# Optimization experiments

Hardware: AMD Instinct MI355X
Metric: run time of the kernel (lower is better)

## Reference

```python
import jax, jax.numpy as jnp
import numpy as np
import math

B, S, D, HD = 8, 2048, 768, 64  # batch, seq, emb_hidden_dim, head_dim


def setup_inputs() -> dict:
    key = jax.random.key(0)
    ks = jax.random.split(key, 7)
    scale_w = 1.0 / math.sqrt(D)
    return {
        "X": jax.random.normal(ks[0], (B, S, D), dtype=jnp.float32),
        "Wq": jax.random.normal(ks[1], (D, HD), dtype=jnp.float32) * scale_w,
        "bq": jax.random.normal(ks[2], (HD,), dtype=jnp.float32) * 0.01,
        "Wk": jax.random.normal(ks[3], (D, HD), dtype=jnp.float32) * scale_w,
        "bk": jax.random.normal(ks[4], (HD,), dtype=jnp.float32) * 0.01,
        "Wv": jax.random.normal(ks[5], (D, HD), dtype=jnp.float32) * scale_w,
        "bv": jax.random.normal(ks[6], (HD,), dtype=jnp.float32) * 0.01,
    }


def reference(X, Wq, bq, Wk, bk, Wv, bv):
    # Projections: [B,S,D] @ [D,HD] -> [B,S,HD]
    Q = X @ Wq + bq
    K = X @ Wk + bk
    V = X @ Wv + bv
    # NOTE: original divides by sqrt(hidden_dim)=sqrt(D), not sqrt(head_dim)
    inv_scale = 1.0 / math.sqrt(D)
    scores = jnp.einsum("bqd,bkd->bqk", Q, K) * inv_scale  # [B,S,S]
    causal = jnp.tril(jnp.ones((S, S), dtype=bool))
    scores = jnp.where(causal, scores, -jnp.inf)
    attn = jax.nn.softmax(scores, axis=-1)
    # dropout p=0.0 (eval/deterministic reference)
    return jnp.einsum("bqk,bkd->bqd", attn, V)  # [B,S,HD]
```

## Files before the change

### kernel.cpp

```cpp
#include <hip/hip_runtime.h>
#include <hip/hip_bf16.h>
#include <math.h>

typedef __attribute__((ext_vector_type(8))) short short8;
typedef __attribute__((ext_vector_type(4))) float f32x4;

#define SS 2048
#define DD 768
#define HDIM 64
#define MM 16384

__device__ __forceinline__ short f2bf(float f) {
    union { float f; unsigned u; } v; v.f = f;
    unsigned r = (v.u + 0x7fffu + ((v.u >> 16) & 1u)) >> 16;
    return (short)r;
}
__device__ __forceinline__ float bf2f(short s) {
    union { float f; unsigned u; } v;
    v.u = ((unsigned)(unsigned short)s) << 16;
    return v.f;
}

__device__ __forceinline__ void gl_lds(const void* g, void* l) {
    __builtin_amdgcn_global_load_lds(
        (const __attribute__((address_space(1))) unsigned*)g,
        (__attribute__((address_space(3))) unsigned*)l, 16, 0, 0);
}

__global__ void prep_w(const float* __restrict__ Wq, const float* __restrict__ Wk,
                       const float* __restrict__ Wv, short* __restrict__ Wt) {
    int idx = blockIdx.x * 256 + threadIdx.x;
    int col = idx / DD;
    int k   = idx - col * DD;
    const float* W = (col < 64) ? Wq : (col < 128) ? Wk : Wv;
    int c = col & 63;
    Wt[idx] = f2bf(W[k * HDIM + c]);
}

__global__ __launch_bounds__(512)
void proj_qkv(const float* __restrict__ X, const short* __restrict__ Wt,
              const float* __restrict__ bq, const float* __restrict__ bk,
              const float* __restrict__ bv,
              short* __restrict__ Qg, short* __restrict__ Kg, short* __restrict__ Vt) {
    __shared__ float Xl[2][2048];
    __shared__ short Wl[2][12288];
    const int tid = threadIdx.x;
    const int w = tid >> 6, lane = tid & 63;
    const int lr = lane & 15, lg = lane >> 4;
    const int wr = w >> 2, wc = w & 3;
    const int row0 = blockIdx.x * 32;

    f32x4 acc[3];
    #pragma unroll
    for (int cf = 0; cf < 3; cf++) acc[cf] = (f32x4)0.0f;

    auto stage = [&](int kk, int buf) {
        {
            int o = w * 1024 + lane * 16;
            int row = o >> 8, ch = (o >> 4) & 15;
            const char* src = (const char*)X + (size_t)(row0 + row) * 3072
                              + kk * 256 + ((ch ^ (row & 7)) << 4);
            gl_lds(src, (char*)&Xl[buf][0] + w * 1024);
        }
        #pragma unroll
        for (int s = 0; s < 3; s++) {
            int i = w * 3 + s;
            int o = i * 1024 + lane * 16;
            int col = o >> 7, ch = (o >> 4) & 7;
            const char* src = (const char*)Wt + (size_t)col * 1536
                              + kk * 128 + ((ch ^ (col & 7)) << 4);
            gl_lds(src, (char*)&Wl[buf][0] + i * 1024);
        }
    };

    stage(0, 0);
    __syncthreads();
    int buf = 0;
    for (int kk = 0; kk < 12; kk++) {
        if (kk < 11) stage(kk + 1, buf ^ 1);
        const char* xb = (const char*)&Xl[buf][0];
        const char* wb = (const char*)&Wl[buf][0];
        #pragma unroll
        for (int ksub = 0; ksub < 2; ksub++) {
            int r = wr * 16 + lr;
            int b0 = r * 256 + ksub * 128 + lg * 32;
            f32x4 x0 = *(const f32x4*)(xb + ((b0)      ^ ((r & 7) << 4)));
            f32x4 x1 = *(const f32x4*)(xb + ((b0 + 16) ^ ((r & 7) << 4)));
            short8 a;
            a[0]=f2bf(x0[0]); a[1]=f2bf(x0[1]); a[2]=f2bf(x0[2]); a[3]=f2bf(x0[3]);
            a[4]=f2bf(x1[0]); a[5]=f2bf(x1[1]); a[6]=f2bf(x1[2]); a[7]=f2bf(x1[3]);
            #pragma unroll
            for (int cf = 0; cf < 3; cf++) {
                int col = wc * 48 + cf * 16 + lr;
                short8 bfr = *(const short8*)(wb +
                    ((col * 128 + ksub * 64 + lg * 16) ^ ((col & 7) << 4)));
                acc[cf] = __builtin_amdgcn_mfma_f32_16x16x32_bf16(a, bfr, acc[cf], 0, 0, 0);
            }
        }
        __syncthreads();
        buf ^= 1;
    }

    #pragma unroll
    for (int cf = 0; cf < 3; cf++) {
        int gcol = wc * 48 + cf * 16 + lr;
        int m = gcol >> 6, cc = gcol & 63;
        float bias = (m == 0 ? bq : m == 1 ? bk : bv)[cc];
        #pragma unroll
        for (int i = 0; i < 4; i++) {
            int r = row0 + wr * 16 + lg * 4 + i;
            short o = f2bf(acc[cf][i] + bias);
            if (m == 0)      Qg[(size_t)r * HDIM + cc] = o;
            else if (m == 1) Kg[(size_t)r * HDIM + cc] = o;
            else             Vt[(size_t)cc * MM + r]   = o;
        }
    }
}

__global__ __launch_bounds__(512)
void attn_part(const short* __restrict__ Qg, const short* __restrict__ Kg,
               const short* __restrict__ Vt,
               short* __restrict__ Opart, float* __restrict__ Ml,
               float* __restrict__ out) {
    __shared__ short Kl[2][4096];
    __shared__ short Vl[2][4096];
    __shared__ short Pl[8][1024];
    const int tid = threadIdx.x;
    const int w = tid >> 6, lane = tid & 63;
    const int lr = lane & 15, lg = lane >> 4;
    const int b = blockIdx.y;

    int idx = 71 - (int)blockIdx.x;
    int g = 0;
    while (idx >= (g + 1) * (g + 2)) g++;
    int rem = idx - g * (g + 1);
    int jq = rem / (g + 1);
    const int J = 2 * g + jq;
    const int c = rem - jq * (g + 1);
    const int t0 = c * 4;
    const int t1 = min(2 * J + 2, t0 + 4);

    const int q0 = J * 128 + w * 16;
    char* plbase = (char*)&Pl[w][0];

    short8 qf[2];
    qf[0] = *(const short8*)(Qg + ((size_t)b * SS + q0 + lr) * HDIM + lg * 8);
    qf[1] = *(const short8*)(Qg + ((size_t)b * SS + q0 + lr) * HDIM + 32 + lg * 8);

    f32x4 oacc[4];
    #pragma unroll
    for (int d = 0; d < 4; d++) oacc[d] = (f32x4)0.0f;
    float mrow[4] = {-INFINITY, -INFINITY, -INFINITY, -INFINITY};
    float lrow[4] = {0.f, 0.f, 0.f, 0.f};
    const float scl = 0.03608439182435161f;

    auto stage = [&](int t, int buf) {
        const int kv0 = t * 64;
        {
            int o = w * 1024 + lane * 16;
            int row = o >> 7, ch = (o >> 4) & 7;
            const char* src = (const char*)Kg + ((size_t)b * SS + kv0) * 128
                              + row * 128 + ((ch ^ (row & 7)) << 4);
            gl_lds(src, (char*)&Kl[buf][0] + w * 1024);
        }
        {
            int o = w * 1024 + lane * 16;
            int col = o >> 7, ch = (o >> 4) & 7;
            const char* src = (const char*)Vt + (size_t)col * (MM * 2)
                              + ((size_t)b * SS + kv0) * 2 + ((ch ^ (col & 7)) << 4);
            gl_lds(src, (char*)&Vl[buf][0] + w * 1024);
        }
    };

    stage(t0, 0);
    __syncthreads();
    int buf = 0;
    for (int t = t0; t < t1; t++) {
        if (t + 1 < t1) stage(t + 1, buf ^ 1);
        const int kv0 = t * 64;
        const bool active = (kv0 <= q0 + 15);
        if (active) {
            const char* kb = (const char*)&Kl[buf][0];
            f32x4 sacc[4];
            #pragma unroll
            for (int ct = 0; ct < 4; ct++) sacc[ct] = (f32x4)0.0f;
            #pragma unroll
            for (int ct = 0; ct < 4; ct++) {
                int row = ct * 16 + lr;
                short8 k0 = *(const short8*)(kb + ((row * 128 +      lg * 16) ^ ((row & 7) << 4)));
                short8 k1 = *(const short8*)(kb + ((row * 128 + 64 + lg * 16) ^ ((row & 7) << 4)));
                sacc[ct] = __builtin_amdgcn_mfma_f32_16x16x32_bf16(qf[0], k0, sacc[ct], 0, 0, 0);
                sacc[ct] = __builtin_amdgcn_mfma_f32_16x16x32_bf16(qf[1], k1, sacc[ct], 0, 0, 0);
            }

            const bool maskt = (kv0 + 63 > q0);
            float p[4][4];
            float rm[4] = {-1e30f, -1e30f, -1e30f, -1e30f};
            #pragma unroll
            for (int ct = 0; ct < 4; ct++) {
                #pragma unroll
                for (int i = 0; i < 4; i++) {
                    float s = sacc[ct][i] * scl;
                    if (maskt) {
                        int kv = kv0 + ct * 16 + lr;
                        int qr = q0 + lg * 4 + i;
                        if (kv > qr) s = -1e30f;
                    }
                    p[ct][i] = s;
                    rm[i] = fmaxf(rm[i], s);
                }
            }
            #pragma unroll
            for (int i = 0; i < 4; i++) {
                float v = rm[i];
                v = fmaxf(v, __shfl_xor(v, 1));
                v = fmaxf(v, __shfl_xor(v, 2));
                v = fmaxf(v, __shfl_xor(v, 4));
                v = fmaxf(v, __shfl_xor(v, 8));
                rm[i] = v;
            }
            float rs[4];
            #pragma unroll
            for (int i = 0; i < 4; i++) {
                float mn = fmaxf(mrow[i], rm[i]);
                float scale = __expf(mrow[i] - mn);
                mrow[i] = mn;
                lrow[i] *= scale;
                for (int d = 0; d < 4; d++) oacc[d][i] *= scale;
                float sum = 0.f;
                #pragma unroll
                for (int ct = 0; ct < 4; ct++) {
                    float e = __expf(p[ct][i] - mn);
                    p[ct][i] = e;
                    sum += e;
                }
                rs[i] = sum;
            }
            #pragma unroll
            for (int i = 0; i < 4; i++) {
                float v = rs[i];
                v += __shfl_xor(v, 1);
                v += __shfl_xor(v, 2);
                v += __shfl_xor(v, 4);
                v += __shfl_xor(v, 8);
                lrow[i] += v;
            }

            #pragma unroll
            for (int ct = 0; ct < 4; ct++) {
                #pragma unroll
                for (int i = 0; i < 4; i++) {
                    int r = lg * 4 + i;
                    int byteoff = r * 128 + (ct * 16 + lr) * 2;
                    *(short*)(plbase + (byteoff ^ ((r & 7) << 4))) = f2bf(p[ct][i]);
                }
            }

            const char* vb = (const char*)&Vl[buf][0];
            #pragma unroll
            for (int ks = 0; ks < 2; ks++) {
                int byteoff = lr * 128 + ks * 64 + lg * 16;
                short8 pf = *(const short8*)(plbase + (byteoff ^ ((lr & 7) << 4)));
                #pragma unroll
                for (int d = 0; d < 4; d++) {
                    int col = d * 16 + lr;
                    short8 vf = *(const short8*)(vb +
                        ((col * 128 + ks * 64 + lg * 16) ^ ((col & 7) << 4)));
                    oacc[d] = __builtin_amdgcn_mfma_f32_16x16x32_bf16(pf, vf, oacc[d], 0, 0, 0);
                }
            }
        }
        __syncthreads();
        buf ^= 1;
    }

    if (J <= 1) {
        #pragma unroll
        for (int d = 0; d < 4; d++)
            #pragma unroll
            for (int i = 0; i < 4; i++)
                out[((size_t)b * SS + q0 + lg * 4 + i) * HDIM + d * 16 + lr]
                    = oacc[d][i] / lrow[i];
    } else {
        const int pb = (b * 16 + J) * 8 + c;
        short* op = Opart + (size_t)pb * 8192 + (size_t)(w * 16) * 64;
        #pragma unroll
        for (int d = 0; d < 4; d++)
            #pragma unroll
            for (int i = 0; i < 4; i++)
                op[(lg * 4 + i) * 64 + d * 16 + lr] = f2bf(oacc[d][i]);
        if (lr == 0) {
            float* ml = Ml + (size_t)pb * 256;
            for (int i = 0; i < 4; i++) {
                ml[w * 16 + lg * 4 + i]       = mrow[i];
                ml[128 + w * 16 + lg * 4 + i] = lrow[i];
            }
        }
    }
}

__global__ __launch_bounds__(256)
void attn_comb(const short* __restrict__ Opart, const float* __restrict__ Ml,
               float* __restrict__ out) {
    const int J = blockIdx.x + 2, b = blockIdx.y;
    const int nc = (J >> 1) + 1;
    const int tid = threadIdx.x;
    const int r = tid >> 1, h = tid & 1;
    const int base = (b * 16 + J) * 8;

    float m = -INFINITY;
    for (int c = 0; c < nc; c++) m = fmaxf(m, Ml[(size_t)(base + c) * 256 + r]);

    float L = 0.f;
    f32x4 acc[8];
    #pragma unroll
    for (int q = 0; q < 8; q++) acc[q] = (f32x4)0.0f;
    for (int c = 0; c < nc; c++) {
        const float* ml = Ml + (size_t)(base + c) * 256;
        float sc = __expf(ml[r] - m);
        L += ml[128 + r] * sc;
        const short* op = Opart + (size_t)(base + c) * 8192 + r * 64 + h * 32;
        #pragma unroll
        for (int q = 0; q < 4; q++) {
            short8 s = *(const short8*)(op + q * 8);
            f32x4 lo = {bf2f(s[0]), bf2f(s[1]), bf2f(s[2]), bf2f(s[3])};
            f32x4 hi = {bf2f(s[4]), bf2f(s[5]), bf2f(s[6]), bf2f(s[7])};
            acc[q * 2]     += lo * sc;
            acc[q * 2 + 1] += hi * sc;
        }
    }
    float inv = 1.0f / L;
    float* o = out + ((size_t)b * SS + J * 128 + r) * HDIM + h * 32;
    #pragma unroll
    for (int q = 0; q < 8; q++) {
        f32x4 v = acc[q] * inv;
        *(f32x4*)(o + q * 4) = v;
    }
}

extern "C" void kernel_launch(void* const* d_in, const int* in_sizes, int n_in,
                              void* d_out, int out_size, void* d_ws, size_t ws_size,
                              hipStream_t stream) {
    const float* X  = (const float*)d_in[0];
    const float* Wq = (const float*)d_in[1];
    const float* bq = (const float*)d_in[2];
    const float* Wk = (const float*)d_in[3];
    const float* bk = (const float*)d_in[4];
    const float* Wv = (const float*)d_in[5];
    const float* bv = (const float*)d_in[6];
    float* out = (float*)d_out;

    char* ws = (char*)d_ws;
    short* Wt = (short*)(ws);
    short* Qg = (short*)(ws + 294912);
    short* Kg = (short*)(ws + 294912 + 2097152);
    short* Vt = (short*)(ws + 294912 + 2 * 2097152);
    size_t opOff = 294912 + 3 * (size_t)2097152;
    short* Op = (short*)(ws + opOff);
    float* Ml = (float*)(ws + opOff + (size_t)1024 * 8192 * 2);

    prep_w<<<576, 256, 0, stream>>>(Wq, Wk, Wv, Wt);
    proj_qkv<<<512, 512, 0, stream>>>(X, Wt, bq, bk, bv, Qg, Kg, Vt);
    attn_part<<<dim3(72, 8), 512, 0, stream>>>(Qg, Kg, Vt, Op, Ml, out);
    attn_comb<<<dim3(14, 8), 256, 0, stream>>>(Op, Ml, out);
}
```

Measured before the change: 59.37 us.

## Triple-buffer projection loads and double rows per block in proj_qkv

The QKV projection kernel now processes 64 rows per block instead of 32, with each wave computing 6 column fragments instead of 3. That halves the grid and halves how often the weight tile is reloaded per output row. The LDS staging moves from double to triple buffering, waiting on vmcnt before a barrier so that two stages stay in flight. This costs more LDS (about 120KB) and more accumulator registers, which may lower occupancy, and with 256 blocks the GPU may be underfilled.

Measured after the change: 63.44 us. +6.8%, slower.

```diff
diff --git a/kernel.cpp b/kernel.cpp
--- a/kernel.cpp
+++ b/kernel.cpp
@@ -9,6 +9,11 @@
 #define DD 768
 #define HDIM 64
 #define MM 16384
+
+#define WAITB(NLIT) do { \
+    asm volatile("s_waitcnt vmcnt(" NLIT ")\n\ts_barrier" ::: "memory"); \
+    __builtin_amdgcn_sched_barrier(0); \
+} while (0)
 
 __device__ __forceinline__ short f2bf(float f) {
     union { float f; unsigned u; } v; v.f = f;
@@ -42,25 +47,27 @@
               const float* __restrict__ bq, const float* __restrict__ bk,
               const float* __restrict__ bv,
               short* __restrict__ Qg, short* __restrict__ Kg, short* __restrict__ Vt) {
-    __shared__ float Xl[2][2048];
-    __shared__ short Wl[2][12288];
+    __shared__ float Xl[3][4096];
+    __shared__ short Wl[3][12288];
     const int tid = threadIdx.x;
     const int w = tid >> 6, lane = tid & 63;
     const int lr = lane & 15, lg = lane >> 4;
-    const int wr = w >> 2, wc = w & 3;
-    const int row0 = blockIdx.x * 32;
-
-    f32x4 acc[3];
-    #pragma unroll
-    for (int cf = 0; cf < 3; cf++) acc[cf] = (f32x4)0.0f;
+    const int wr = w >> 1, wc = w & 1;
+    const int row0 = blockIdx.x * 64;
+
+    f32x4 acc[6];
+    #pragma unroll
+    for (int cf = 0; cf < 6; cf++) acc[cf] = (f32x4)0.0f;
 
     auto stage = [&](int kk, int buf) {
-        {
-            int o = w * 1024 + lane * 16;
+        #pragma unroll
+        for (int s = 0; s < 2; s++) {
+            int i = w * 2 + s;
+            int o = i * 1024 + lane * 16;
             int row = o >> 8, ch = (o >> 4) & 15;
             const char* src = (const char*)X + (size_t)(row0 + row) * 3072
                               + kk * 256 + ((ch ^ (row & 7)) << 4);
-            gl_lds(src, (char*)&Xl[buf][0] + w * 1024);
+            gl_lds(src, (char*)&Xl[buf][0] + i * 1024);
         }
         #pragma unroll
         for (int s = 0; s < 3; s++) {
@@ -74,12 +81,14 @@
     };
 
     stage(0, 0);
-    __syncthreads();
-    int buf = 0;
-    for (int kk = 0; kk < 12; kk++) {
-        if (kk < 11) stage(kk + 1, buf ^ 1);
-        const char* xb = (const char*)&Xl[buf][0];
-        const char* wb = (const char*)&Wl[buf][0];
+    stage(1, 1);
+    int bc = 0, bs = 2;
+    for (int t = 0; t < 12; t++) {
+        if (t < 11) { WAITB("5"); }
+        else        { WAITB("0"); }
+        if (t < 10) stage(t + 2, bs);
+        const char* xb = (const char*)&Xl[bc][0];
+        const char* wb = (const char*)&Wl[bc][0];
         #pragma unroll
         for (int ksub = 0; ksub < 2; ksub++) {
             int r = wr * 16 + lr;
@@ -90,20 +99,20 @@
             a[0]=f2bf(x0[0]); a[1]=f2bf(x0[1]); a[2]=f2bf(x0[2]); a[3]=f2bf(x0[3]);
             a[4]=f2bf(x1[0]); a[5]=f2bf(x1[1]); a[6]=f2bf(x1[2]); a[7]=f2bf(x1[3]);
             #pragma unroll
-            for (int cf = 0; cf < 3; cf++) {
-                int col = wc * 48 + cf * 16 + lr;
+            for (int cf = 0; cf < 6; cf++) {
+                int col = wc * 96 + cf * 16 + lr;
                 short8 bfr = *(const short8*)(wb +
                     ((col * 128 + ksub * 64 + lg * 16) ^ ((col & 7) << 4)));
                 acc[cf] = __builtin_amdgcn_mfma_f32_16x16x32_bf16(a, bfr, acc[cf], 0, 0, 0);
             }
         }
-        __syncthreads();
-        buf ^= 1;
-    }
-
-    #pragma unroll
-    for (int cf = 0; cf < 3; cf++) {
-        int gcol = wc * 48 + cf * 16 + lr;
+        bc = (bc == 2) ? 0 : bc + 1;
+        bs = (bs == 2) ? 0 : bs + 1;
+    }
+
+    #pragma unroll
+    for (int cf = 0; cf < 6; cf++) {
+        int gcol = wc * 96 + cf * 16 + lr;
         int m = gcol >> 6, cc = gcol & 63;
         float bias = (m == 0 ? bq : m == 1 ? bk : bv)[cc];
         #pragma unroll
@@ -360,7 +369,7 @@
     float* Ml = (float*)(ws + opOff + (size_t)1024 * 8192 * 2);
 
     prep_w<<<576, 256, 0, stream>>>(Wq, Wk, Wv, Wt);
-    proj_qkv<<<512, 512, 0, stream>>>(X, Wt, bq, bk, bv, Qg, Kg, Vt);
+    proj_qkv<<<256, 512, 0, stream>>>(X, Wt, bq, bk, bv, Qg, Kg, Vt);
     attn_part<<<dim3(72, 8), 512, 0, stream>>>(Qg, Kg, Vt, Op, Ml, out);
     attn_comb<<<dim3(14, 8), 256, 0, stream>>>(Op, Ml, out);
 }
```

## Enlarge attention query tile to 256 rows with two row-tiles per wave

Applied to the files above, without the earlier changes.

Each attention block now covers 256 query rows, with every wave handling two 16-row tiles, and each block processes 2 KV tiles instead of up to 4. Each staged K/V tile in LDS is therefore reused across twice as many query rows, which cuts global K/V traffic per unit of work. Every block now writes partials, including those for the first query block, so the combine kernel always runs, over 8 groups of 256 rows. The cost is more register pressure from doubled accumulators, plus larger partial buffers and combine work that now covers all rows.

After: 81.77 us. 1.38x slower.

```diff
diff --git a/kernel.cpp b/kernel.cpp
--- a/kernel.cpp
+++ b/kernel.cpp
@@ -120,8 +120,7 @@
 __global__ __launch_bounds__(512)
 void attn_part(const short* __restrict__ Qg, const short* __restrict__ Kg,
                const short* __restrict__ Vt,
-               short* __restrict__ Opart, float* __restrict__ Ml,
-               float* __restrict__ out) {
+               short* __restrict__ Opart, float* __restrict__ Ml) {
     __shared__ short Kl[2][4096];
     __shared__ short Vl[2][4096];
     __shared__ short Pl[8][1024];
@@ -133,25 +132,31 @@
     int idx = 71 - (int)blockIdx.x;
     int g = 0;
     while (idx >= (g + 1) * (g + 2)) g++;
-    int rem = idx - g * (g + 1);
-    int jq = rem / (g + 1);
-    const int J = 2 * g + jq;
-    const int c = rem - jq * (g + 1);
-    const int t0 = c * 4;
-    const int t1 = min(2 * J + 2, t0 + 4);
-
-    const int q0 = J * 128 + w * 16;
+    const int c = idx - g * (g + 1);
+    const int t0 = 2 * c;
+    const int t1 = min(4 * g + 4, 2 * c + 2);
+
+    const int q0 = g * 256 + w * 32;
     char* plbase = (char*)&Pl[w][0];
 
-    short8 qf[2];
-    qf[0] = *(const short8*)(Qg + ((size_t)b * SS + q0 + lr) * HDIM + lg * 8);
-    qf[1] = *(const short8*)(Qg + ((size_t)b * SS + q0 + lr) * HDIM + 32 + lg * 8);
-
-    f32x4 oacc[4];
-    #pragma unroll
-    for (int d = 0; d < 4; d++) oacc[d] = (f32x4)0.0f;
-    float mrow[4] = {-INFINITY, -INFINITY, -INFINITY, -INFINITY};
-    float lrow[4] = {0.f, 0.f, 0.f, 0.f};
+    short8 qf[2][2];
+    #pragma unroll
+    for (int rt = 0; rt < 2; rt++) {
+        const short* qp = Qg + ((size_t)b * SS + q0 + rt * 16 + lr) * HDIM + lg * 8;
+        qf[rt][0] = *(const short8*)(qp);
+        qf[rt][1] = *(const short8*)(qp + 32);
+    }
+
+    f32x4 oacc[2][4];
+    float mrow[2][4], lrow[2][4];
+    #pragma unroll
+    for (int rt = 0; rt < 2; rt++)
+        #pragma unroll
+        for (int d = 0; d < 4; d++) {
+            oacc[rt][d] = (f32x4)0.0f;
+            mrow[rt][d] = -INFINITY;
+            lrow[rt][d] = 0.f;
+        }
     const float scl = 0.03608439182435161f;
 
     auto stage = [&](int t, int buf) {
@@ -178,95 +183,98 @@
     for (int t = t0; t < t1; t++) {
         if (t + 1 < t1) stage(t + 1, buf ^ 1);
         const int kv0 = t * 64;
-        const bool active = (kv0 <= q0 + 15);
-        if (active) {
-            const char* kb = (const char*)&Kl[buf][0];
-            f32x4 sacc[4];
-            #pragma unroll
-            for (int ct = 0; ct < 4; ct++) sacc[ct] = (f32x4)0.0f;
-            #pragma unroll
-            for (int ct = 0; ct < 4; ct++) {
-                int row = ct * 16 + lr;
-                short8 k0 = *(const short8*)(kb + ((row * 128 +      lg * 16) ^ ((row & 7) << 4)));
-                short8 k1 = *(const short8*)(kb + ((row * 128 + 64 + lg * 16) ^ ((row & 7) << 4)));
-                sacc[ct] = __builtin_amdgcn_mfma_f32_16x16x32_bf16(qf[0], k0, sacc[ct], 0, 0, 0);
-                sacc[ct] = __builtin_amdgcn_mfma_f32_16x16x32_bf16(qf[1], k1, sacc[ct], 0, 0, 0);
-            }
-
-            const bool maskt = (kv0 + 63 > q0);
-            float p[4][4];
-            float rm[4] = {-1e30f, -1e30f, -1e30f, -1e30f};
-            #pragma unroll
-            for (int ct = 0; ct < 4; ct++) {
+        const char* kb = (const char*)&Kl[buf][0];
+        const char* vb = (const char*)&Vl[buf][0];
+        #pragma unroll
+        for (int rt = 0; rt < 2; rt++) {
+            const int qr0 = q0 + rt * 16;
+            if (kv0 <= qr0 + 15) {
+                f32x4 sacc[4];
+                #pragma unroll
+                for (int ct = 0; ct < 4; ct++) sacc[ct] = (f32x4)0.0f;
+                #pragma unroll
+                for (int ct = 0; ct < 4; ct++) {
+                    int row = ct * 16 + lr;
+                    short8 k0 = *(const short8*)(kb + ((row * 128 +      lg * 16) ^ ((row & 7) << 4)));
+                    short8 k1 = *(const short8*)(kb + ((row * 128 + 64 + lg * 16) ^ ((row & 7) << 4)));
+                    sacc[ct] = __builtin_amdgcn_mfma_f32_16x16x32_bf16(qf[rt][0], k0, sacc[ct], 0, 0, 0);
+                    sacc[ct] = __builtin_amdgcn_mfma_f32_16x16x32_bf16(qf[rt][1], k1, sacc[ct], 0, 0, 0);
+                }
+
+                const bool maskt = (kv0 + 63 > qr0);
+                float p[4][4];
+                float rm[4] = {-1e30f, -1e30f, -1e30f, -1e30f};
+                #pragma unroll
+                for (int ct = 0; ct < 4; ct++) {
+                    #pragma unroll
+                    for (int i = 0; i < 4; i++) {
+                        float s = sacc[ct][i] * scl;
+                        if (maskt) {
+                            int kv = kv0 + ct * 16 + lr;
+                            int qr = qr0 + lg * 4 + i;
+                            if (kv > qr) s = -1e30f;
+                        }
+                        p[ct][i] = s;
+                        rm[i] = fmaxf(rm[i], s);
+                    }
+                }
                 #pragma unroll
                 for (int i = 0; i < 4; i++) {
-                    float s = sacc[ct][i] * scl;
-                    if (maskt) {
-                        int kv = kv0 + ct * 16 + lr;
-                        int qr = q0 + lg * 4 + i;
-                        if (kv > qr) s = -1e30f;
+                    float v = rm[i];
+                    v = fmaxf(v, __shfl_xor(v, 1));
+                    v = fmaxf(v, __shfl_xor(v, 2));
+                    v = fmaxf(v, __shfl_xor(v, 4));
+                    v = fmaxf(v, __shfl_xor(v, 8));
+                    rm[i] = v;
+                }
+                float rs[4];
+                #pragma unroll
+                for (int i = 0; i < 4; i++) {
+                    float mn = fmaxf(mrow[rt][i], rm[i]);
+                    float scale = __expf(mrow[rt][i] - mn);
+                    mrow[rt][i] = mn;
+                    lrow[rt][i] *= scale;
+                    for (int d = 0; d < 4; d++) oacc[rt][d][i] *= scale;
+                    float sum = 0.f;
+                    #pragma unroll
+                    for (int ct = 0; ct < 4; ct++) {
+                        float e = __expf(p[ct][i] - mn);
+                        p[ct][i] = e;
+                        sum += e;
                     }
-                    p[ct][i] = s;
-                    rm[i] = fmaxf(rm[i], s);
-                }
-            }
-            #pragma unroll
-            for (int i = 0; i < 4; i++) {
-                float v = rm[i];
-                v = fmaxf(v, __shfl_xor(v, 1));
-                v = fmaxf(v, __shfl_xor(v, 2));
-                v = fmaxf(v, __shfl_xor(v, 4));
-                v = fmaxf(v, __shfl_xor(v, 8));
-                rm[i] = v;
-            }
-            float rs[4];
-            #pragma unroll
-            for (int i = 0; i < 4; i++) {
-                float mn = fmaxf(mrow[i], rm[i]);
-                float scale = __expf(mrow[i] - mn);
-                mrow[i] = mn;
-                lrow[i] *= scale;
-                for (int d = 0; d < 4; d++) oacc[d][i] *= scale;
-                float sum = 0.f;
+                    rs[i] = sum;
+                }
+                #pragma unroll
+                for (int i = 0; i < 4; i++) {
+                    float v = rs[i];
+                    v += __shfl_xor(v, 1);
+                    v += __shfl_xor(v, 2);
+                    v += __shfl_xor(v, 4);
+                    v += __shfl_xor(v, 8);
+                    lrow[rt][i] += v;
+                }
+
                 #pragma unroll
                 for (int ct = 0; ct < 4; ct++) {
-                    float e = __expf(p[ct][i] - mn);
-                    p[ct][i] = e;
-                    sum += e;
-                }
-                rs[i] = sum;
-            }
-            #pragma unroll
-            for (int i = 0; i < 4; i++) {
-                float v = rs[i];
-                v += __shfl_xor(v, 1);
-                v += __shfl_xor(v, 2);
-                v += __shfl_xor(v, 4);
-                v += __shfl_xor(v, 8);
-                lrow[i] += v;
-            }
-
-            #pragma unroll
-            for (int ct = 0; ct < 4; ct++) {
-                #pragma unroll
-                for (int i = 0; i < 4; i++) {
-                    int r = lg * 4 + i;
-                    int byteoff = r * 128 + (ct * 16 + lr) * 2;
-                    *(short*)(plbase + (byteoff ^ ((r & 7) << 4))) = f2bf(p[ct][i]);
-                }
-            }
-
-            const char* vb = (const char*)&Vl[buf][0];
-            #pragma unroll
-            for (int ks = 0; ks < 2; ks++) {
-                int byteoff = lr * 128 + ks * 64 + lg * 16;
-                short8 pf = *(const short8*)(plbase + (byteoff ^ ((lr & 7) << 4)));
-                #pragma unroll
-                for (int d = 0; d < 4; d++) {
-                    int col = d * 16 + lr;
-                    short8 vf = *(const short8*)(vb +
-                        ((col * 128 + ks * 64 + lg * 16) ^ ((col & 7) << 4)));
-                    oacc[d] = __builtin_amdgcn_mfma_f32_16x16x32_bf16(pf, vf, oacc[d], 0, 0, 0);
+                    #pragma unroll
+                    for (int i = 0; i < 4; i++) {
+                        int r = lg * 4 + i;
+                        int byteoff = r * 128 + (ct * 16 + lr) * 2;
+                        *(short*)(plbase + (byteoff ^ ((r & 7) << 4))) = f2bf(p[ct][i]);
+                    }
+                }
+
+                #pragma unroll
+                for (int ks = 0; ks < 2; ks++) {
+                    int byteoff = lr * 128 + ks * 64 + lg * 16;
+                    short8 pf = *(const short8*)(plbase + (byteoff ^ ((lr & 7) << 4)));
+                    #pragma unroll
+                    for (int d = 0; d < 4; d++) {
+                        int col = d * 16 + lr;
+                        short8 vf = *(const short8*)(vb +
+                            ((col * 128 + ks * 64 + lg * 16) ^ ((col & 7) << 4)));
+                        oacc[rt][d] = __builtin_amdgcn_mfma_f32_16x16x32_bf16(pf, vf, oacc[rt][d], 0, 0, 0);
+                    }
                 }
             }
         }
@@ -274,54 +282,48 @@
         buf ^= 1;
     }
 
-    if (J <= 1) {
+    const int pb = (b * 8 + g) * 16 + c;
+    short* op = Opart + (size_t)pb * 16384 + (size_t)(w * 32) * 64;
+    #pragma unroll
+    for (int rt = 0; rt < 2; rt++)
         #pragma unroll
         for (int d = 0; d < 4; d++)
             #pragma unroll
             for (int i = 0; i < 4; i++)
-                out[((size_t)b * SS + q0 + lg * 4 + i) * HDIM + d * 16 + lr]
-                    = oacc[d][i] / lrow[i];
-    } else {
-        const int pb = (b * 16 + J) * 8 + c;
-        short* op = Opart + (size_t)pb * 8192 + (size_t)(w * 16) * 64;
-        #pragma unroll
-        for (int d = 0; d < 4; d++)
-            #pragma unroll
-            for (int i = 0; i < 4; i++)
-                op[(lg * 4 + i) * 64 + d * 16 + lr] = f2bf(oacc[d][i]);
-        if (lr == 0) {
-            float* ml = Ml + (size_t)pb * 256;
+                op[(rt * 16 + lg * 4 + i) * 64 + d * 16 + lr] = f2bf(oacc[rt][d][i]);
+    if (lr == 0) {
+        float* ml = Ml + (size_t)pb * 512;
+        #pragma unroll
+        for (int rt = 0; rt < 2; rt++)
             for (int i = 0; i < 4; i++) {
-                ml[w * 16 + lg * 4 + i]       = mrow[i];
-                ml[128 + w * 16 + lg * 4 + i] = lrow[i];
+                ml[w * 32 + rt * 16 + lg * 4 + i]       = mrow[rt][i];
+                ml[256 + w * 32 + rt * 16 + lg * 4 + i] = lrow[rt][i];
             }
-        }
     }
 }
 
 __global__ __launch_bounds__(256)
 void attn_comb(const short* __restrict__ Opart, const float* __restrict__ Ml,
                float* __restrict__ out) {
-    const int J = blockIdx.x + 2, b = blockIdx.y;
-    const int nc = (J >> 1) + 1;
-    const int tid = threadIdx.x;
-    const int r = tid >> 1, h = tid & 1;
-    const int base = (b * 16 + J) * 8;
+    const int g = blockIdx.x, b = blockIdx.y;
+    const int nc = 2 * g + 2;
+    const int r = threadIdx.x;
+    const int base = (b * 8 + g) * 16;
 
     float m = -INFINITY;
-    for (int c = 0; c < nc; c++) m = fmaxf(m, Ml[(size_t)(base + c) * 256 + r]);
+    for (int c = 0; c < nc; c++) m = fmaxf(m, Ml[(size_t)(base + c) * 512 + r]);
 
     float L = 0.f;
-    f32x4 acc[8];
-    #pragma unroll
-    for (int q = 0; q < 8; q++) acc[q] = (f32x4)0.0f;
+    f32x4 acc[16];
+    #pragma unroll
+    for (int q = 0; q < 16; q++) acc[q] = (f32x4)0.0f;
     for (int c = 0; c < nc; c++) {
-        const float* ml = Ml + (size_t)(base + c) * 256;
+        const float* ml = Ml + (size_t)(base + c) * 512;
         float sc = __expf(ml[r] - m);
-        L += ml[128 + r] * sc;
-        const short* op = Opart + (size_t)(base + c) * 8192 + r * 64 + h * 32;
-        #pragma unroll
-        for (int q = 0; q < 4; q++) {
+        L += ml[256 + r] * sc;
+        const short* op = Opart + (size_t)(base + c) * 16384 + r * 64;
+        #pragma unroll
+        for (int q = 0; q < 8; q++) {
             short8 s = *(const short8*)(op + q * 8);
             f32x4 lo = {bf2f(s[0]), bf2f(s[1]), bf2f(s[2]), bf2f(s[3])};
             f32x4 hi = {bf2f(s[4]), bf2f(s[5]), bf2f(s[6]), bf2f(s[7])};
@@ -330,9 +332,9 @@
         }
     }
     float inv = 1.0f / L;
-    float* o = out + ((size_t)b * SS + J * 128 + r) * HDIM + h * 32;
-    #pragma unroll
-    for (int q = 0; q < 8; q++) {
+    float* o = out + ((size_t)b * SS + g * 256 + r) * HDIM;
+    #pragma unroll
+    for (int q = 0; q < 16; q++) {
         f32x4 v = acc[q] * inv;
         *(f32x4*)(o + q * 4) = v;
     }
@@ -357,10 +359,10 @@
     short* Vt = (short*)(ws + 294912 + 2 * 2097152);
     size_t opOff = 294912 + 3 * (size_t)2097152;
     short* Op = (short*)(ws + opOff);
-    float* Ml = (float*)(ws + opOff + (size_t)1024 * 8192 * 2);
+    float* Ml = (float*)(ws + opOff + (size_t)1024 * 16384 * 2);
 
     prep_w<<<576, 256, 0, stream>>>(Wq, Wk, Wv, Wt);
     proj_qkv<<<512, 512, 0, stream>>>(X, Wt, bq, bk, bv, Qg, Kg, Vt);
-    attn_part<<<dim3(72, 8), 512, 0, stream>>>(Qg, Kg, Vt, Op, Ml, out);
-    attn_comb<<<dim3(14, 8), 256, 0, stream>>>(Op, Ml, out);
-}
+    attn_part<<<dim3(72, 8), 512, 0, stream>>>(Qg, Kg, Vt, Op, Ml);
+    attn_comb<<<dim3(8, 8), 256, 0, stream>>>(Op, Ml, out);
+}
```

## Load K/V straight from global memory and split KV into finer chunks

Applied to the files above, without the earlier changes.

Removes the LDS double-buffered K/V staging and its barriers, so each wave reads K and V fragments directly from global memory (relying on L2/L1 caching). It also halves the KV chunk size per block (2 tiles instead of 4), which raises the attention grid from 72 to 136 blocks per batch and doubles the number of partial results the combine kernel must merge. Each wave now also clips its own loop to its causal limit instead of idling behind a block-wide barrier. The risk is uncoalesced and redundant global reads, since all 8 waves fetch the same K/V, plus more partial-output traffic. The workspace must also be large enough for the doubled partial buffer.

Result: slower. 88.61 us (+49.2%).

```diff
diff --git a/kernel.cpp b/kernel.cpp
--- a/kernel.cpp
+++ b/kernel.cpp
@@ -122,25 +122,20 @@
                const short* __restrict__ Vt,
                short* __restrict__ Opart, float* __restrict__ Ml,
                float* __restrict__ out) {
-    __shared__ short Kl[2][4096];
-    __shared__ short Vl[2][4096];
     __shared__ short Pl[8][1024];
     const int tid = threadIdx.x;
     const int w = tid >> 6, lane = tid & 63;
     const int lr = lane & 15, lg = lane >> 4;
     const int b = blockIdx.y;
 
-    int idx = 71 - (int)blockIdx.x;
-    int g = 0;
-    while (idx >= (g + 1) * (g + 2)) g++;
-    int rem = idx - g * (g + 1);
-    int jq = rem / (g + 1);
-    const int J = 2 * g + jq;
-    const int c = rem - jq * (g + 1);
-    const int t0 = c * 4;
-    const int t1 = min(2 * J + 2, t0 + 4);
+    int idx = 135 - (int)blockIdx.x;
+    int J = 0;
+    while (idx >= (J + 1) * (J + 2) / 2) J++;
+    const int c = idx - J * (J + 1) / 2;
+    const int t0 = 2 * c;
 
     const int q0 = J * 128 + w * 16;
+    const int tmax = min(2 * c + 2, ((q0 + 15) >> 6) + 1);
     char* plbase = (char*)&Pl[w][0];
 
     short8 qf[2];
@@ -154,127 +149,99 @@
     float lrow[4] = {0.f, 0.f, 0.f, 0.f};
     const float scl = 0.03608439182435161f;
 
-    auto stage = [&](int t, int buf) {
+    for (int t = t0; t < tmax; t++) {
         const int kv0 = t * 64;
-        {
-            int o = w * 1024 + lane * 16;
-            int row = o >> 7, ch = (o >> 4) & 7;
-            const char* src = (const char*)Kg + ((size_t)b * SS + kv0) * 128
-                              + row * 128 + ((ch ^ (row & 7)) << 4);
-            gl_lds(src, (char*)&Kl[buf][0] + w * 1024);
-        }
-        {
-            int o = w * 1024 + lane * 16;
-            int col = o >> 7, ch = (o >> 4) & 7;
-            const char* src = (const char*)Vt + (size_t)col * (MM * 2)
-                              + ((size_t)b * SS + kv0) * 2 + ((ch ^ (col & 7)) << 4);
-            gl_lds(src, (char*)&Vl[buf][0] + w * 1024);
-        }
-    };
-
-    stage(t0, 0);
-    __syncthreads();
-    int buf = 0;
-    for (int t = t0; t < t1; t++) {
-        if (t + 1 < t1) stage(t + 1, buf ^ 1);
-        const int kv0 = t * 64;
-        const bool active = (kv0 <= q0 + 15);
-        if (active) {
-            const char* kb = (const char*)&Kl[buf][0];
-            f32x4 sacc[4];
-            #pragma unroll
-            for (int ct = 0; ct < 4; ct++) sacc[ct] = (f32x4)0.0f;
+        const short* kp = Kg + ((size_t)b * SS + kv0) * HDIM;
+        f32x4 sacc[4];
+        #pragma unroll
+        for (int ct = 0; ct < 4; ct++) sacc[ct] = (f32x4)0.0f;
+        #pragma unroll
+        for (int ct = 0; ct < 4; ct++) {
+            const short* kpc = kp + (size_t)(ct * 16 + lr) * HDIM + lg * 8;
+            short8 k0 = *(const short8*)(kpc);
+            short8 k1 = *(const short8*)(kpc + 32);
+            sacc[ct] = __builtin_amdgcn_mfma_f32_16x16x32_bf16(qf[0], k0, sacc[ct], 0, 0, 0);
+            sacc[ct] = __builtin_amdgcn_mfma_f32_16x16x32_bf16(qf[1], k1, sacc[ct], 0, 0, 0);
+        }
+
+        const bool maskt = (kv0 + 63 > q0);
+        float p[4][4];
+        float rm[4] = {-1e30f, -1e30f, -1e30f, -1e30f};
+        #pragma unroll
+        for (int ct = 0; ct < 4; ct++) {
+            #pragma unroll
+            for (int i = 0; i < 4; i++) {
+                float s = sacc[ct][i] * scl;
+                if (maskt) {
+                    int kv = kv0 + ct * 16 + lr;
+                    int qr = q0 + lg * 4 + i;
+                    if (kv > qr) s = -1e30f;
+                }
+                p[ct][i] = s;
+                rm[i] = fmaxf(rm[i], s);
+            }
+        }
+        #pragma unroll
+        for (int i = 0; i < 4; i++) {
+            float v = rm[i];
+            v = fmaxf(v, __shfl_xor(v, 1));
+            v = fmaxf(v, __shfl_xor(v, 2));
+            v = fmaxf(v, __shfl_xor(v, 4));
+            v = fmaxf(v, __shfl_xor(v, 8));
+            rm[i] = v;
+        }
+        float rs[4];
+        #pragma unroll
+        for (int i = 0; i < 4; i++) {
+            float mn = fmaxf(mrow[i], rm[i]);
+            float scale = __expf(mrow[i] - mn);
+            mrow[i] = mn;
+            lrow[i] *= scale;
+            for (int d = 0; d < 4; d++) oacc[d][i] *= scale;
+            float sum = 0.f;
             #pragma unroll
             for (int ct = 0; ct < 4; ct++) {
-                int row = ct * 16 + lr;
-                short8 k0 = *(const short8*)(kb + ((row * 128 +      lg * 16) ^ ((row & 7) << 4)));
-                short8 k1 = *(const short8*)(kb + ((row * 128 + 64 + lg * 16) ^ ((row & 7) << 4)));
-                sacc[ct] = __builtin_amdgcn_mfma_f32_16x16x32_bf16(qf[0], k0, sacc[ct], 0, 0, 0);
-                sacc[ct] = __builtin_amdgcn_mfma_f32_16x16x32_bf16(qf[1], k1, sacc[ct], 0, 0, 0);
-            }
-
-            const bool maskt = (kv0 + 63 > q0);
-            float p[4][4];
-            float rm[4] = {-1e30f, -1e30f, -1e30f, -1e30f};
-            #pragma unroll
-            for (int ct = 0; ct < 4; ct++) {
-                #pragma unroll
-                for (int i = 0; i < 4; i++) {
-                    float s = sacc[ct][i] * scl;
-                    if (maskt) {
-                        int kv = kv0 + ct * 16 + lr;
-                        int qr = q0 + lg * 4 + i;
-                        if (kv > qr) s = -1e30f;
-                    }
-                    p[ct][i] = s;
-                    rm[i] = fmaxf(rm[i], s);
-                }
-            }
+                float e = __expf(p[ct][i] - mn);
+                p[ct][i] = e;
+                sum += e;
+            }
+            rs[i] = sum;
+        }
+        #pragma unroll
+        for (int i = 0; i < 4; i++) {
+            float v = rs[i];
+            v += __shfl_xor(v, 1);
+            v += __shfl_xor(v, 2);
+            v += __shfl_xor(v, 4);
+            v += __shfl_xor(v, 8);
+            lrow[i] += v;
+        }
+
+        #pragma unroll
+        for (int ct = 0; ct < 4; ct++) {
             #pragma unroll
             for (int i = 0; i < 4; i++) {
-                float v = rm[i];
-                v = fmaxf(v, __shfl_xor(v, 1));
-                v = fmaxf(v, __shfl_xor(v, 2));
-                v = fmaxf(v, __shfl_xor(v, 4));
-                v = fmaxf(v, __shfl_xor(v, 8));
-                rm[i] = v;
-            }
-            float rs[4];
-            #pragma unroll
-            for (int i = 0; i < 4; i++) {
-                float mn = fmaxf(mrow[i], rm[i]);
-                float scale = __expf(mrow[i] - mn);
-                mrow[i] = mn;
-                lrow[i] *= scale;
-                for (int d = 0; d < 4; d++) oacc[d][i] *= scale;
-                float sum = 0.f;
-                #pragma unroll
-                for (int ct = 0; ct < 4; ct++) {
-                    float e = __expf(p[ct][i] - mn);
-                    p[ct][i] = e;
-                    sum += e;
-                }
-                rs[i] = sum;
-            }
-            #pragma unroll
-            for (int i = 0; i < 4; i++) {
-                float v = rs[i];
-                v += __shfl_xor(v, 1);
-                v += __shfl_xor(v, 2);
-                v += __shfl_xor(v, 4);
-                v += __shfl_xor(v, 8);
-                lrow[i] += v;
-            }
-
-            #pragma unroll
-            for (int ct = 0; ct < 4; ct++) {
-                #pragma unroll
-                for (int i = 0; i < 4; i++) {
-                    int r = lg * 4 + i;
-                    int byteoff = r * 128 + (ct * 16 + lr) * 2;
-                    *(short*)(plbase + (byteoff ^ ((r & 7) << 4))) = f2bf(p[ct][i]);
-                }
-            }
-
-            const char* vb = (const char*)&Vl[buf][0];
-            #pragma unroll
-            for (int ks = 0; ks < 2; ks++) {
-                int byteoff = lr * 128 + ks * 64 + lg * 16;
-                short8 pf = *(const short8*)(plbase + (byteoff ^ ((lr & 7) << 4)));
-                #pragma unroll
-                for (int d = 0; d < 4; d++) {
-                    int col = d * 16 + lr;
-                    short8 vf = *(const short8*)(vb +
-                        ((col * 128 + ks * 64 + lg * 16) ^ ((col & 7) << 4)));
-                    oacc[d] = __builtin_amdgcn_mfma_f32_16x16x32_bf16(pf, vf, oacc[d], 0, 0, 0);
-                }
-            }
-        }
-        __syncthreads();
-        buf ^= 1;
-    }
-
-    if (J <= 1) {
+                int r = lg * 4 + i;
+                int byteoff = r * 128 + (ct * 16 + lr) * 2;
+                *(short*)(plbase + (byteoff ^ ((r & 7) << 4))) = f2bf(p[ct][i]);
+            }
+        }
+
+        const short* vp = Vt + (size_t)b * SS + kv0;
+        #pragma unroll
+        for (int ks = 0; ks < 2; ks++) {
+            int byteoff = lr * 128 + ks * 64 + lg * 16;
+            short8 pf = *(const short8*)(plbase + (byteoff ^ ((lr & 7) << 4)));
+            #pragma unroll
+            for (int d = 0; d < 4; d++) {
+                const short* vpc = vp + (size_t)(d * 16 + lr) * MM + ks * 32 + lg * 8;
+                short8 vf = *(const short8*)vpc;
+                oacc[d] = __builtin_amdgcn_mfma_f32_16x16x32_bf16(pf, vf, oacc[d], 0, 0, 0);
+            }
+        }
+    }
+
+    if (J == 0) {
         #pragma unroll
         for (int d = 0; d < 4; d++)
             #pragma unroll
@@ -282,7 +249,7 @@
                 out[((size_t)b * SS + q0 + lg * 4 + i) * HDIM + d * 16 + lr]
                     = oacc[d][i] / lrow[i];
     } else {
-        const int pb = (b * 16 + J) * 8 + c;
+        const int pb = (b * 16 + J) * 16 + c;
         short* op = Opart + (size_t)pb * 8192 + (size_t)(w * 16) * 64;
         #pragma unroll
         for (int d = 0; d < 4; d++)
@@ -302,11 +269,11 @@
 __global__ __launch_bounds__(256)
 void attn_comb(const short* __restrict__ Opart, const float* __restrict__ Ml,
                float* __restrict__ out) {
-    const int J = blockIdx.x + 2, b = blockIdx.y;
-    const int nc = (J >> 1) + 1;
+    const int J = blockIdx.x + 1, b = blockIdx.y;
+    const int nc = J + 1;
     const int tid = threadIdx.x;
     const int r = tid >> 1, h = tid & 1;
-    const int base = (b * 16 + J) * 8;
+    const int base = (b * 16 + J) * 16;
 
     float m = -INFINITY;
     for (int c = 0; c < nc; c++) m = fmaxf(m, Ml[(size_t)(base + c) * 256 + r]);
@@ -357,10 +324,10 @@
     short* Vt = (short*)(ws + 294912 + 2 * 2097152);
     size_t opOff = 294912 + 3 * (size_t)2097152;
     short* Op = (short*)(ws + opOff);
-    float* Ml = (float*)(ws + opOff + (size_t)1024 * 8192 * 2);
+    float* Ml = (float*)(ws + opOff + (size_t)2048 * 8192 * 2);
 
     prep_w<<<576, 256, 0, stream>>>(Wq, Wk, Wv, Wt);
     proj_qkv<<<512, 512, 0, stream>>>(X, Wt, bq, bk, bv, Qg, Kg, Vt);
-    attn_part<<<dim3(72, 8), 512, 0, stream>>>(Qg, Kg, Vt, Op, Ml, out);
-    attn_comb<<<dim3(14, 8), 256, 0, stream>>>(Op, Ml, out);
-}
+    attn_part<<<dim3(136, 8), 512, 0, stream>>>(Qg, Kg, Vt, Op, Ml, out);
+    attn_comb<<<dim3(15, 8), 256, 0, stream>>>(Op, Ml, out);
+}
```
